# Optimization experiments

Measured on AMD Instinct MI355X. Metric: run time of the kernel, lower is better.

Reference implementation:

```python
import jax, jax.numpy as jnp
import numpy as np

K_HIDDEN = 512
N_POS = 24
N_COLOR = 6
EPS = 1e-5


def setup_inputs() -> dict:
    key = jax.random.key(0)
    k1, k2 = jax.random.split(key)
    B = 1024
    x = jax.random.normal(k1, (B, N_POS, N_COLOR * K_HIDDEN), dtype=jnp.float32)
    # kaiming-uniform-ish scale for the (k_out, k_in, 2) weight
    fan_in = K_HIDDEN * 2
    bound = float(np.sqrt(6.0 / fan_in))
    conv_weight = jax.random.uniform(k2, (K_HIDDEN, K_HIDDEN, 2), dtype=jnp.float32,
                                     minval=-bound, maxval=bound)
    conv_bias = jnp.zeros((K_HIDDEN,), dtype=jnp.float32)
    norm_weight = jnp.ones((K_HIDDEN,), dtype=jnp.float32)
    norm_bias = jnp.zeros((K_HIDDEN,), dtype=jnp.float32)
    return {"x": x, "conv_weight": conv_weight, "conv_bias": conv_bias,
            "norm_weight": norm_weight, "norm_bias": norm_bias}


def _color_layernorm(x, gamma, beta):
    # x: (B, 24, 6*k); normalize over the full channel axis, affine tied per block of 6
    mean = jnp.mean(x, axis=-1, keepdims=True)
    var = jnp.mean(jnp.square(x - mean), axis=-1, keepdims=True)  # unbiased=False
    xn = (x - mean) * jax.lax.rsqrt(var + EPS)
    xn = xn.reshape(*x.shape[:-1], K_HIDDEN, N_COLOR)
    xn = xn * gamma[:, None] + beta[:, None]
    return xn.reshape(x.shape)


def _color_conv(x, weight, bias):
    # x: (B, 24, 6*k) -> (B, 24, k, 6)
    B = x.shape[0]
    xr = x.reshape(B, N_POS, K_HIDDEN, N_COLOR)
    alpha = weight[:, :, 0] - weight[:, :, 1]   # (k_out, k_in)
    beta_w = weight[:, :, 1]                    # (k_out, k_in)
    term1 = jnp.einsum('bikd,ok->biod', xr, alpha)      # per-color linear
    x_sum = xr.sum(axis=3)                               # (B, 24, k_in)
    term2 = jnp.einsum('bik,ok->bio', x_sum, beta_w)     # color-sum linear
    out = term1 + term2[..., None] + bias[None, None, :, None]
    return out.reshape(B, N_POS, K_HIDDEN * N_COLOR)


def reference(x, conv_weight, conv_bias, norm_weight, norm_bias):
    h = _color_layernorm(x, norm_weight, norm_bias)
    h = _color_conv(h, conv_weight, conv_bias)
    return x + jax.nn.relu(h)
```

## Files before the change

kernel.cpp:

```cpp
#include <hip/hip_runtime.h>
#include <stdint.h>
#include <stddef.h>

#define KH   512
#define DF   3072
#define EPSF 1e-5f
#define PPB  8
#define ROWS 48
#define TSS  516

typedef __attribute__((ext_vector_type(4))) float f32x4;
typedef __attribute__((ext_vector_type(2))) float f32x2;
typedef __attribute__((ext_vector_type(8))) short bf16x8;
typedef __attribute__((ext_vector_type(4))) unsigned int u32x4;

__device__ __forceinline__ unsigned short f2bf(float f) {
  union { float f; unsigned u; } c; c.f = f;
  unsigned u = c.u;
  u += 0x7fffu + ((u >> 16) & 1u);
  return (unsigned short)(u >> 16);
}
__device__ __forceinline__ unsigned short f2bf_trunc(float f) {
  union { float f; unsigned u; } c; c.f = f;
  return (unsigned short)(c.u >> 16);
}
__device__ __forceinline__ float bf2f(unsigned short u) {
  union { unsigned u; float f; } c; c.u = ((unsigned)u) << 16;
  return c.f;
}
__device__ __forceinline__ float bfl(unsigned u) {
  union { unsigned u; float f; } c; c.u = u << 16;
  return c.f;
}
__device__ __forceinline__ float bfh(unsigned u) {
  union { unsigned u; float f; } c; c.u = u & 0xffff0000u;
  return c.f;
}

__global__ __launch_bounds__(256) void prep_w(const float* __restrict__ cw,
                                              const float* __restrict__ cb,
                                              const float* __restrict__ nw,
                                              const float* __restrict__ nb,
                                              unsigned char* __restrict__ wbt,
                                              float* __restrict__ c12) {
  const int o = blockIdx.x;
  const int t = threadIdx.x;
  const int wn = o >> 6, nn = (o >> 4) & 3, co = o & 15;
  float c1 = 0.f, c2 = 0.f;
  for (int k = t; k < KH; k += 256) {
    float w0 = cw[o * 1024 + 2 * k];
    float w1 = cw[o * 1024 + 2 * k + 1];
    float a  = w0 - w1;
    float g  = nw[k], b = nb[k];
    int s = k >> 5, kin = k & 31, h = kin >> 3, e = kin & 7;
    size_t base = (size_t)(((wn * 16 + s) * 4 + nn)) * 1024 + (h * 16 + co) * 16 + e * 2;
    *(unsigned short*)(wbt + base)          = f2bf(a * g);
    *(unsigned short*)(wbt + base + 524288) = f2bf(w1 * g);
    float tt = a + 6.f * w1;
    c1 += tt * b;
    c2 += tt * g;
  }
  #pragma unroll
  for (int off = 32; off >= 1; off >>= 1) {
    c1 += __shfl_xor(c1, off);
    c2 += __shfl_xor(c2, off);
  }
  __shared__ float s1[4], s2[4];
  int wid = t >> 6, lane = t & 63;
  if (lane == 0) { s1[wid] = c1; s2[wid] = c2; }
  __syncthreads();
  if (t == 0) {
    c12[o]      = s1[0] + s1[1] + s1[2] + s1[3] + cb[o];
    c12[KH + o] = s2[0] + s2[1] + s2[2] + s2[3];
  }
}

__global__ __launch_bounds__(512, 4) void fused_main(
    const float* __restrict__ x,
    const unsigned char* __restrict__ wbt,
    const float* __restrict__ c12,
    float* __restrict__ out)
{
  __shared__ unsigned char As[ROWS * 1024];
  __shared__ unsigned char Sx[PPB * 1024];
  __shared__ float Ts[PPB * TSS];
  __shared__ float st[PPB * 2];

  const int tid  = threadIdx.x;
  const int lane = tid & 63;
  const int wid  = tid >> 6;
  const int co   = lane & 15;
  const int h    = lane >> 4;
  const int rvb  = h << 2;
  const size_t r0 = (size_t)blockIdx.x * PPB;

  float C1r[4], C2r[4];
  #pragma unroll
  for (int n = 0; n < 4; n++) {
    int o = wid * 64 + n * 16 + co;
    C1r[n] = c12[o];
    C2r[n] = c12[KH + o];
  }

  const unsigned char* wA = wbt + (size_t)wid * 65536;
  bf16x8 bvA[4], bvB[4];

  {
    const float* xb = x + r0 * DF;
    f32x4 q[12];
    #pragma unroll
    for (int i = 0; i < 12; i++) q[i] = *(const f32x4*)(xb + i * 2048 + tid * 4);

    #pragma unroll
    for (int n = 0; n < 4; n++)
      bvA[n] = *(const bf16x8*)(wA + n * 1024 + lane * 16);

    #pragma unroll
    for (int i = 0; i < 12; i++) {
      int base = i * 2048 + tid * 4;
      int pl   = base / 3072;
      int rem  = base - pl * 3072;
      int k0   = rem / 6;
      int d0   = rem - k0 * 6;
      #pragma unroll
      for (int e = 0; e < 4; e++) {
        int d = d0 + e, k = k0;
        if (d >= 6) { d -= 6; k += 1; }
        int row  = pl * 6 + d;
        int byte = row * 1024 + ((((k >> 3) ^ (row & 7)) << 4)) + (k & 7) * 2;
        *(unsigned short*)(As + byte) = f2bf_trunc(q[i][e]);
      }
    }
  }
  __syncthreads();

  {
    float vals[48];
    #pragma unroll
    for (int d = 0; d < 6; d++) {
      int row = wid * 6 + d;
      u32x4 v = *(const u32x4*)(As + row * 1024 + ((lane ^ (row & 7)) << 4));
      #pragma unroll
      for (int jj = 0; jj < 4; jj++) {
        vals[d * 8 + 2 * jj]     = bfl(v[jj]);
        vals[d * 8 + 2 * jj + 1] = bfh(v[jj]);
      }
    }
    float s = 0.f, sq = 0.f;
    #pragma unroll
    for (int i = 0; i < 48; i++) { s += vals[i]; sq += vals[i] * vals[i]; }
    #pragma unroll
    for (int off = 32; off >= 1; off >>= 1) {
      s  += __shfl_xor(s,  off);
      sq += __shfl_xor(sq, off);
    }
    float mean = s * (1.f / 3072.f);
    float var  = sq * (1.f / 3072.f) - mean * mean;
    float rstd = rsqrtf(var + EPSF);
    if (lane == 0) { st[2 * wid] = mean; st[2 * wid + 1] = rstd; }
    bf16x8 sv;
    #pragma unroll
    for (int g = 0; g < 8; g++) {
      float ss = vals[g] + vals[8 + g] + vals[16 + g] + vals[24 + g] +
                 vals[32 + g] + vals[40 + g];
      sv[g] = (short)f2bf(ss);
    }
    *(bf16x8*)(Sx + wid * 1024 + ((lane ^ (wid & 7)) << 4)) = sv;
  }
  __syncthreads();

  f32x4 acc1[3][4];
  #pragma unroll
  for (int m = 0; m < 3; m++)
    #pragma unroll
    for (int n = 0; n < 4; n++) acc1[m][n] = (f32x4){0.f, 0.f, 0.f, 0.f};

  int arow[3], ar7[3];
  #pragma unroll
  for (int m = 0; m < 3; m++) {
    int row = m * 16 + co;
    arow[m] = row * 1024;  ar7[m] = row & 7;
  }

  {
    #pragma unroll 1
    for (int s = 0; s < 16; s += 2) {
      const unsigned char* pn = wA + (size_t)(s + 1) * 4096;
      #pragma unroll
      for (int n = 0; n < 4; n++)
        bvB[n] = *(const bf16x8*)(pn + n * 1024 + lane * 16);
      {
        int g6 = s * 4 + h;
        bf16x8 af[3];
        #pragma unroll
        for (int m = 0; m < 3; m++)
          af[m] = *(const bf16x8*)(As + arow[m] + ((g6 ^ ar7[m]) << 4));
        #pragma unroll
        for (int m = 0; m < 3; m++)
          #pragma unroll
          for (int n = 0; n < 4; n++)
            acc1[m][n] = __builtin_amdgcn_mfma_f32_16x16x32_bf16(af[m], bvA[n], acc1[m][n], 0, 0, 0);
      }
      if (s + 2 < 16) {
        const unsigned char* pn2 = wA + (size_t)(s + 2) * 4096;
        #pragma unroll
        for (int n = 0; n < 4; n++)
          bvA[n] = *(const bf16x8*)(pn2 + n * 1024 + lane * 16);
      }
      {
        int g6 = (s + 1) * 4 + h;
        bf16x8 af[3];
        #pragma unroll
        for (int m = 0; m < 3; m++)
          af[m] = *(const bf16x8*)(As + arow[m] + ((g6 ^ ar7[m]) << 4));
        #pragma unroll
        for (int m = 0; m < 3; m++)
          #pragma unroll
          for (int n = 0; n < 4; n++)
            acc1[m][n] = __builtin_amdgcn_mfma_f32_16x16x32_bf16(af[m], bvB[n], acc1[m][n], 0, 0, 0);
      }
    }
  }

  {
    f32x4 acc2[4];
    #pragma unroll
    for (int n = 0; n < 4; n++) acc2[n] = (f32x4){0.f, 0.f, 0.f, 0.f};
    const unsigned char* wB2 = wbt + 524288 + (size_t)wid * 65536;
    const int sxr = (co & 7);
    bf16x8 cA[4], cB[4];
    #pragma unroll
    for (int n = 0; n < 4; n++)
      cA[n] = *(const bf16x8*)(wB2 + n * 1024 + lane * 16);
    #pragma unroll 1
    for (int s = 0; s < 16; s += 2) {
      const unsigned char* pn = wB2 + (size_t)(s + 1) * 4096;
      #pragma unroll
      for (int n = 0; n < 4; n++)
        cB[n] = *(const bf16x8*)(pn + n * 1024 + lane * 16);
      {
        int g6 = s * 4 + h;
        bf16x8 a2 = *(const bf16x8*)(Sx + sxr * 1024 + ((g6 ^ sxr) << 4));
        #pragma unroll
        for (int n = 0; n < 4; n++)
          acc2[n] = __builtin_amdgcn_mfma_f32_16x16x32_bf16(a2, cA[n], acc2[n], 0, 0, 0);
      }
      if (s + 2 < 16) {
        const unsigned char* pn2 = wB2 + (size_t)(s + 2) * 4096;
        #pragma unroll
        for (int n = 0; n < 4; n++)
          cA[n] = *(const bf16x8*)(pn2 + n * 1024 + lane * 16);
      }
      {
        int g6 = (s + 1) * 4 + h;
        bf16x8 a2 = *(const bf16x8*)(Sx + sxr * 1024 + ((g6 ^ sxr) << 4));
        #pragma unroll
        for (int n = 0; n < 4; n++)
          acc2[n] = __builtin_amdgcn_mfma_f32_16x16x32_bf16(a2, cB[n], acc2[n], 0, 0, 0);
      }
    }
    if (h < 2) {
      #pragma unroll
      for (int n = 0; n < 4; n++)
        #pragma unroll
        for (int v = 0; v < 4; v++)
          Ts[(rvb + v) * TSS + wid * 64 + n * 16 + co] = acc2[n][v];
    }
  }

  #pragma unroll
  for (int n = 0; n < 4; n++) {
    const int o = wid * 64 + n * 16 + co;
    const int swzo = o >> 3;
    const int ob2 = (o & 7) * 2;
    #pragma unroll
    for (int m = 0; m < 3; m++) {
      int j0  = m * 16 + rvb;
      int pl0 = j0 / 6;
      int d0  = j0 - pl0 * 6;
      float mean0 = st[2 * pl0], rstd0 = st[2 * pl0 + 1];
      float t20   = Ts[pl0 * TSS + o];
      float cc0   = C1r[n] - mean0 * rstd0 * C2r[n];
      if (d0 < 3) {
        f32x4 ov;
        #pragma unroll
        for (int v = 0; v < 4; v++) {
          int j = j0 + v;
          unsigned short rx = *(const unsigned short*)(
              As + j * 1024 + ((swzo ^ (j & 7)) << 4) + ob2);
          ov[v] = bf2f(rx) + fmaxf(rstd0 * (acc1[m][n][v] + t20) + cc0, 0.f);
        }
        *(f32x4*)(out + (r0 + pl0) * DF + o * 6 + d0) = ov;
      } else {
        int pl1 = pl0 + 1;
        float mean1 = st[2 * pl1], rstd1 = st[2 * pl1 + 1];
        float t21   = Ts[pl1 * TSS + o];
        float cc1   = C1r[n] - mean1 * rstd1 * C2r[n];
        f32x2 o0, o1;
        #pragma unroll
        for (int v = 0; v < 2; v++) {
          int j = j0 + v;
          unsigned short rx = *(const unsigned short*)(
              As + j * 1024 + ((swzo ^ (j & 7)) << 4) + ob2);
          o0[v] = bf2f(rx) + fmaxf(rstd0 * (acc1[m][n][v] + t20) + cc0, 0.f);
        }
        #pragma unroll
        for (int v = 2; v < 4; v++) {
          int j = j0 + v;
          unsigned short rx = *(const unsigned short*)(
              As + j * 1024 + ((swzo ^ (j & 7)) << 4) + ob2);
          o1[v - 2] = bf2f(rx) + fmaxf(rstd1 * (acc1[m][n][v] + t21) + cc1, 0.f);
        }
        *(f32x2*)(out + (r0 + pl0) * DF + o * 6 + 4) = o0;
        *(f32x2*)(out + (r0 + pl1) * DF + o * 6)     = o1;
      }
    }
  }
}

extern "C" void kernel_launch(void* const* d_in, const int* in_sizes, int n_in,
                              void* d_out, int out_size, void* d_ws, size_t ws_size,
                              hipStream_t stream) {
  (void)n_in; (void)out_size; (void)ws_size;
  const float* x  = (const float*)d_in[0];
  const float* cw = (const float*)d_in[1];
  const float* cb = (const float*)d_in[2];
  const float* nw = (const float*)d_in[3];
  const float* nb = (const float*)d_in[4];
  float* out = (float*)d_out;

  unsigned char* wbt = (unsigned char*)d_ws;
  float* c12 = (float*)((char*)d_ws + (size_t)1024 * 1024);

  prep_w<<<512, 256, 0, stream>>>(cw, cb, nw, nb, wbt, c12);

  const int R = in_sizes[0] / DF;
  fused_main<<<R / PPB, 512, 0, stream>>>(x, wbt, c12, out);
}
```

Baseline: 241.2 us.

## Double block to 1024 threads, halving output columns per wave

Each block now runs 16 waves instead of 8. Every wave owns 32 output channels instead of 64, so per-wave MFMA accumulators and weight registers are halved. The weight prefetch is simplified from a two-buffer ping-pong to a single buffer reloaded after each step. The layernorm-stats phase is restricted to the first 8 waves. This aims to raise occupancy and latency hiding, but each wave does fewer MFMAs per A-fragment load, and the weaker prefetch may expose more global-load latency.

```diff
diff --git a/kernel.cpp b/kernel.cpp
--- a/kernel.cpp
+++ b/kernel.cpp
@@ -75,7 +75,7 @@
   }
 }
 
-__global__ __launch_bounds__(512, 4) void fused_main(
+__global__ __launch_bounds__(1024, 8) void fused_main(
     const float* __restrict__ x,
     const unsigned char* __restrict__ wbt,
     const float* __restrict__ c12,
@@ -94,30 +94,31 @@
   const int rvb  = h << 2;
   const size_t r0 = (size_t)blockIdx.x * PPB;
 
-  float C1r[4], C2r[4];
-  #pragma unroll
-  for (int n = 0; n < 4; n++) {
-    int o = wid * 64 + n * 16 + co;
+  float C1r[2], C2r[2];
+  #pragma unroll
+  for (int n = 0; n < 2; n++) {
+    int o = wid * 32 + n * 16 + co;
     C1r[n] = c12[o];
     C2r[n] = c12[KH + o];
   }
 
-  const unsigned char* wA = wbt + (size_t)wid * 65536;
-  bf16x8 bvA[4], bvB[4];
+  const size_t wAoff = ((size_t)(wid >> 1) * 65536) + ((size_t)(wid & 1) * 2048)
+                     + (size_t)lane * 16;
+  bf16x8 bv[2];
 
   {
     const float* xb = x + r0 * DF;
-    f32x4 q[12];
-    #pragma unroll
-    for (int i = 0; i < 12; i++) q[i] = *(const f32x4*)(xb + i * 2048 + tid * 4);
-
-    #pragma unroll
-    for (int n = 0; n < 4; n++)
-      bvA[n] = *(const bf16x8*)(wA + n * 1024 + lane * 16);
-
-    #pragma unroll
-    for (int i = 0; i < 12; i++) {
-      int base = i * 2048 + tid * 4;
+    f32x4 q[6];
+    #pragma unroll
+    for (int i = 0; i < 6; i++) q[i] = *(const f32x4*)(xb + i * 4096 + tid * 4);
+
+    #pragma unroll
+    for (int n = 0; n < 2; n++)
+      bv[n] = *(const bf16x8*)(wbt + wAoff + n * 1024);
+
+    #pragma unroll
+    for (int i = 0; i < 6; i++) {
+      int base = i * 4096 + tid * 4;
       int pl   = base / 3072;
       int rem  = base - pl * 3072;
       int k0   = rem / 6;
@@ -134,7 +135,7 @@
   }
   __syncthreads();
 
-  {
+  if (wid < 8) {
     float vals[48];
     #pragma unroll
     for (int d = 0; d < 6; d++) {
@@ -169,11 +170,11 @@
   }
   __syncthreads();
 
-  f32x4 acc1[3][4];
+  f32x4 acc1[3][2];
   #pragma unroll
   for (int m = 0; m < 3; m++)
     #pragma unroll
-    for (int n = 0; n < 4; n++) acc1[m][n] = (f32x4){0.f, 0.f, 0.f, 0.f};
+    for (int n = 0; n < 2; n++) acc1[m][n] = (f32x4){0.f, 0.f, 0.f, 0.f};
 
   int arow[3], ar7[3];
   #pragma unroll
@@ -182,95 +183,59 @@
     arow[m] = row * 1024;  ar7[m] = row & 7;
   }
 
+  #pragma unroll 1
+  for (int s = 0; s < 16; s++) {
+    int g6 = s * 4 + h;
+    bf16x8 af[3];
+    #pragma unroll
+    for (int m = 0; m < 3; m++)
+      af[m] = *(const bf16x8*)(As + arow[m] + ((g6 ^ ar7[m]) << 4));
+    #pragma unroll
+    for (int m = 0; m < 3; m++)
+      #pragma unroll
+      for (int n = 0; n < 2; n++)
+        acc1[m][n] = __builtin_amdgcn_mfma_f32_16x16x32_bf16(af[m], bv[n], acc1[m][n], 0, 0, 0);
+    if (s + 1 < 16) {
+      #pragma unroll
+      for (int n = 0; n < 2; n++)
+        bv[n] = *(const bf16x8*)(wbt + wAoff + (size_t)(s + 1) * 4096 + n * 1024);
+    }
+  }
+
   {
+    f32x4 acc2[2];
+    acc2[0] = (f32x4){0.f, 0.f, 0.f, 0.f};
+    acc2[1] = (f32x4){0.f, 0.f, 0.f, 0.f};
+    const int sxr = (co & 7);
+    bf16x8 cA[2];
+    #pragma unroll
+    for (int n = 0; n < 2; n++)
+      cA[n] = *(const bf16x8*)(wbt + 524288 + wAoff + n * 1024);
     #pragma unroll 1
-    for (int s = 0; s < 16; s += 2) {
-      const unsigned char* pn = wA + (size_t)(s + 1) * 4096;
-      #pragma unroll
-      for (int n = 0; n < 4; n++)
-        bvB[n] = *(const bf16x8*)(pn + n * 1024 + lane * 16);
-      {
-        int g6 = s * 4 + h;
-        bf16x8 af[3];
-        #pragma unroll
-        for (int m = 0; m < 3; m++)
-          af[m] = *(const bf16x8*)(As + arow[m] + ((g6 ^ ar7[m]) << 4));
-        #pragma unroll
-        for (int m = 0; m < 3; m++)
-          #pragma unroll
-          for (int n = 0; n < 4; n++)
-            acc1[m][n] = __builtin_amdgcn_mfma_f32_16x16x32_bf16(af[m], bvA[n], acc1[m][n], 0, 0, 0);
+    for (int s = 0; s < 16; s++) {
+      int g6 = s * 4 + h;
+      bf16x8 a2 = *(const bf16x8*)(Sx + sxr * 1024 + ((g6 ^ sxr) << 4));
+      #pragma unroll
+      for (int n = 0; n < 2; n++)
+        acc2[n] = __builtin_amdgcn_mfma_f32_16x16x32_bf16(a2, cA[n], acc2[n], 0, 0, 0);
+      if (s + 1 < 16) {
+        #pragma unroll
+        for (int n = 0; n < 2; n++)
+          cA[n] = *(const bf16x8*)(wbt + 524288 + wAoff + (size_t)(s + 1) * 4096 + n * 1024);
       }
-      if (s + 2 < 16) {
-        const unsigned char* pn2 = wA + (size_t)(s + 2) * 4096;
-        #pragma unroll
-        for (int n = 0; n < 4; n++)
-          bvA[n] = *(const bf16x8*)(pn2 + n * 1024 + lane * 16);
-      }
-      {
-        int g6 = (s + 1) * 4 + h;
-        bf16x8 af[3];
-        #pragma unroll
-        for (int m = 0; m < 3; m++)
-          af[m] = *(const bf16x8*)(As + arow[m] + ((g6 ^ ar7[m]) << 4));
-        #pragma unroll
-        for (int m = 0; m < 3; m++)
-          #pragma unroll
-          for (int n = 0; n < 4; n++)
-            acc1[m][n] = __builtin_amdgcn_mfma_f32_16x16x32_bf16(af[m], bvB[n], acc1[m][n], 0, 0, 0);
-      }
-    }
-  }
-
-  {
-    f32x4 acc2[4];
-    #pragma unroll
-    for (int n = 0; n < 4; n++) acc2[n] = (f32x4){0.f, 0.f, 0.f, 0.f};
-    const unsigned char* wB2 = wbt + 524288 + (size_t)wid * 65536;
-    const int sxr = (co & 7);
-    bf16x8 cA[4], cB[4];
-    #pragma unroll
-    for (int n = 0; n < 4; n++)
-      cA[n] = *(const bf16x8*)(wB2 + n * 1024 + lane * 16);
-    #pragma unroll 1
-    for (int s = 0; s < 16; s += 2) {
-      const unsigned char* pn = wB2 + (size_t)(s + 1) * 4096;
-      #pragma unroll
-      for (int n = 0; n < 4; n++)
-        cB[n] = *(const bf16x8*)(pn + n * 1024 + lane * 16);
-      {
-        int g6 = s * 4 + h;
-        bf16x8 a2 = *(const bf16x8*)(Sx + sxr * 1024 + ((g6 ^ sxr) << 4));
-        #pragma unroll
-        for (int n = 0; n < 4; n++)
-          acc2[n] = __builtin_amdgcn_mfma_f32_16x16x32_bf16(a2, cA[n], acc2[n], 0, 0, 0);
-      }
-      if (s + 2 < 16) {
-        const unsigned char* pn2 = wB2 + (size_t)(s + 2) * 4096;
-        #pragma unroll
-        for (int n = 0; n < 4; n++)
-          cA[n] = *(const bf16x8*)(pn2 + n * 1024 + lane * 16);
-      }
-      {
-        int g6 = (s + 1) * 4 + h;
-        bf16x8 a2 = *(const bf16x8*)(Sx + sxr * 1024 + ((g6 ^ sxr) << 4));
-        #pragma unroll
-        for (int n = 0; n < 4; n++)
-          acc2[n] = __builtin_amdgcn_mfma_f32_16x16x32_bf16(a2, cB[n], acc2[n], 0, 0, 0);
-      }
     }
     if (h < 2) {
       #pragma unroll
-      for (int n = 0; n < 4; n++)
+      for (int n = 0; n < 2; n++)
         #pragma unroll
         for (int v = 0; v < 4; v++)
-          Ts[(rvb + v) * TSS + wid * 64 + n * 16 + co] = acc2[n][v];
-    }
-  }
-
-  #pragma unroll
-  for (int n = 0; n < 4; n++) {
-    const int o = wid * 64 + n * 16 + co;
+          Ts[(rvb + v) * TSS + wid * 32 + n * 16 + co] = acc2[n][v];
+    }
+  }
+
+  #pragma unroll
+  for (int n = 0; n < 2; n++) {
+    const int o = wid * 32 + n * 16 + co;
     const int swzo = o >> 3;
     const int ob2 = (o & 7) * 2;
     #pragma unroll
@@ -335,5 +300,5 @@
   prep_w<<<512, 256, 0, stream>>>(cw, cb, nw, nb, wbt, c12);
 
   const int R = in_sizes[0] / DF;
-  fused_main<<<R / PPB, 512, 0, stream>>>(x, wbt, c12, out);
-}
+  fused_main<<<R / PPB, 1024, 0, stream>>>(x, wbt, c12, out);
+}
```

After: 289.5 us. 1.2x slower.
